# Optimization experiments

Measured on AMD Instinct MI355X. Metric: run time of the kernel, lower is better.

The kernel has to match this reference:

```python
import jax, jax.numpy as jnp
import numpy as np

EPS = 1e-5

def setup_inputs() -> dict:
    key = jax.random.key(0)
    kx, kq, kp = jax.random.split(key, 3)
    B, T, d = 4, 4096, 512
    x = jax.random.normal(kx, (B, T, d), dtype=jnp.float32)
    mask = jnp.tril(jnp.ones((T, T), dtype=jnp.int32))  # causal 0/1 mask
    gamma = jnp.ones((d,), dtype=jnp.float32)
    beta = jnp.zeros((d,), dtype=jnp.float32)
    Wqkv = jax.random.normal(kq, (d, 3 * d), dtype=jnp.float32) / np.sqrt(d)
    Wproj = jax.random.normal(kp, (d, d), dtype=jnp.float32) / np.sqrt(d)
    return {"x": x, "mask": mask, "gamma": gamma, "beta": beta, "Wqkv": Wqkv, "Wproj": Wproj}

def reference(x, mask, gamma, beta, Wqkv, Wproj):
    B, T, C = x.shape
    # LayerNorm over last dim
    mu = jnp.mean(x, axis=-1, keepdims=True)
    var = jnp.mean(jnp.square(x - mu), axis=-1, keepdims=True)
    xn = (x - mu) * jax.lax.rsqrt(var + EPS) * gamma + beta
    # QKV projection (no bias)
    qkv = xn @ Wqkv  # [B,T,3C]
    q, k, v = jnp.split(qkv, 3, axis=-1)
    scale = 1.0 / np.sqrt(C)
    dist = jnp.einsum('btc,bsc->bts', q, k) * scale  # [B,T,T]
    dist = jnp.where(mask[:T, :T] == 0, -jnp.inf, dist)
    attn = jax.nn.softmax(dist, axis=-1)
    out = jnp.einsum('bts,bsc->btc', attn, v)
    return out @ Wproj
```

## Files before the change

kernel.cpp:

```cpp
#include <hip/hip_runtime.h>

typedef short bf16x8 __attribute__((ext_vector_type(8)));
typedef float f32x4 __attribute__((ext_vector_type(4)));

#define AS1 __attribute__((address_space(1)))
#define AS3 __attribute__((address_space(3)))

__device__ __forceinline__ void async16(const void* g, void* l) {
    __builtin_amdgcn_global_load_lds((AS1 unsigned*)(unsigned long long)g,
                                     (AS3 unsigned*)l, 16, 0, 0);
}

__device__ __forceinline__ unsigned short f2bf(float f) {
    unsigned u = __builtin_bit_cast(unsigned, f);
    u += 0x7fffu + ((u >> 16) & 1u);
    return (unsigned short)(u >> 16);
}
__device__ __forceinline__ float bf2f(unsigned short s) {
    unsigned u = ((unsigned)s) << 16;
    return __builtin_bit_cast(float, u);
}

__global__ __launch_bounds__(256) void ln_bf16_kernel(
    const float* __restrict__ x, const float* __restrict__ gamma,
    const float* __restrict__ beta, unsigned short* __restrict__ xn, int nrows)
{
    int row = blockIdx.x * 4 + (threadIdx.x >> 6);
    int lane = threadIdx.x & 63;
    if (row >= nrows) return;
    const float4* xr = (const float4*)(x + (size_t)row * 512);
    float4 a = xr[lane], b = xr[lane + 64];
    float s = a.x + a.y + a.z + a.w + b.x + b.y + b.z + b.w;
    #pragma unroll
    for (int m = 1; m < 64; m <<= 1) s += __shfl_xor(s, m);
    float mu = s * (1.0f / 512.0f);
    float dx[8] = {a.x - mu, a.y - mu, a.z - mu, a.w - mu,
                   b.x - mu, b.y - mu, b.z - mu, b.w - mu};
    float ss = 0.f;
    #pragma unroll
    for (int i = 0; i < 8; ++i) ss += dx[i] * dx[i];
    #pragma unroll
    for (int m = 1; m < 64; m <<= 1) ss += __shfl_xor(ss, m);
    float rstd = rsqrtf(ss * (1.0f / 512.0f) + 1e-5f);
    const float4* gp = (const float4*)gamma;
    const float4* bp = (const float4*)beta;
    float4 g0 = gp[lane], g1 = gp[lane + 64], b0 = bp[lane], b1 = bp[lane + 64];
    float y[8];
    y[0] = dx[0] * rstd * g0.x + b0.x; y[1] = dx[1] * rstd * g0.y + b0.y;
    y[2] = dx[2] * rstd * g0.z + b0.z; y[3] = dx[3] * rstd * g0.w + b0.w;
    y[4] = dx[4] * rstd * g1.x + b1.x; y[5] = dx[5] * rstd * g1.y + b1.y;
    y[6] = dx[6] * rstd * g1.z + b1.z; y[7] = dx[7] * rstd * g1.w + b1.w;
    ushort4* orow = (ushort4*)(xn + (size_t)row * 512);
    orow[lane]      = make_ushort4(f2bf(y[0]), f2bf(y[1]), f2bf(y[2]), f2bf(y[3]));
    orow[lane + 64] = make_ushort4(f2bf(y[4]), f2bf(y[5]), f2bf(y[6]), f2bf(y[7]));
}

__global__ __launch_bounds__(256) void transpose_w(
    const float* __restrict__ in, unsigned short* __restrict__ outT, int R, int Cd)
{
    __shared__ float tile[64][65];
    int r0 = blockIdx.x * 64, c0 = blockIdx.y * 64;
    int lr = threadIdx.x >> 6, lc = threadIdx.x & 63;
    #pragma unroll
    for (int i = 0; i < 16; ++i) {
        int r = i * 4 + lr;
        tile[r][lc] = in[(size_t)(r0 + r) * Cd + c0 + lc];
    }
    __syncthreads();
    #pragma unroll
    for (int i = 0; i < 16; ++i) {
        int r = i * 4 + lr;
        outT[(size_t)(c0 + r) * R + r0 + lc] = f2bf(tile[lc][r]);
    }
}

__global__ __launch_bounds__(256) void transpose_v(
    const unsigned short* __restrict__ vraw, unsigned short* __restrict__ vtp)
{
    __shared__ unsigned short tile[64][72];
    int b = blockIdx.z;
    int t0 = blockIdx.x * 64, c0 = blockIdx.y * 64;
    int lr = threadIdx.x >> 6, lc = threadIdx.x & 63;
    const unsigned short* src = vraw + (size_t)(b * 4096 + t0) * 512 + c0;
    #pragma unroll
    for (int i = 0; i < 16; ++i) {
        int r = i * 4 + lr;
        tile[r][lc] = src[(size_t)r * 512 + lc];
    }
    __syncthreads();
    #pragma unroll
    for (int i = 0; i < 16; ++i) {
        int r = i * 4 + lr;
        int c = c0 + r;
        int jt = (t0 >> 5) + (lc >> 5);
        int tl = lc & 31;
        int x = tl >> 3;
        int slot = c * 4 + ((x ^ (c >> 1)) & 3);
        vtp[((size_t)(b * 128 + jt)) * 16384 + slot * 8 + (tl & 7)] = tile[lc][r];
    }
}

__global__ __launch_bounds__(256) void gemm_bt(
    const unsigned short* __restrict__ A, const unsigned short* __restrict__ Bt,
    void* __restrict__ Cp, int M, int N, int K, int lda, int ldb, int ldc, int outBf16)
{
    __shared__ unsigned short As[128 * 64];
    __shared__ unsigned short Bs[128 * 64];
    const int tid = threadIdx.x;
    const int w = tid >> 6, lane = tid & 63, quad = lane >> 4, l15 = lane & 15;
    const int wm = w >> 1, wn = w & 1;
    const size_t m0 = (size_t)blockIdx.x * 128, n0 = (size_t)blockIdx.y * 128;
    f32x4 zero = {0.f, 0.f, 0.f, 0.f};
    f32x4 acc[4][4];
    #pragma unroll
    for (int i = 0; i < 4; ++i)
        #pragma unroll
        for (int j = 0; j < 4; ++j) acc[i][j] = zero;

    for (int k0 = 0; k0 < K; k0 += 64) {
        __syncthreads();
        #pragma unroll
        for (int r = 0; r < 4; ++r) {
            int s = r * 256 + w * 64 + lane;
            int row = s >> 3, x = s & 7, g = x ^ (row & 7);
            async16(A + (m0 + row) * lda + k0 + g * 8,
                    (char*)As + (size_t)(r * 256 + w * 64) * 16);
        }
        #pragma unroll
        for (int r = 0; r < 4; ++r) {
            int s = r * 256 + w * 64 + lane;
            int row = s >> 3, x = s & 7, g = x ^ (row & 7);
            async16(Bt + (n0 + row) * ldb + k0 + g * 8,
                    (char*)Bs + (size_t)(r * 256 + w * 64) * 16);
        }
        __syncthreads();
        #pragma unroll
        for (int ks = 0; ks < 2; ++ks) {
            bf16x8 af[4], bf[4];
            int cc = ks * 4 + quad;
            #pragma unroll
            for (int mt = 0; mt < 4; ++mt) {
                int row = wm * 64 + mt * 16 + l15;
                int x = cc ^ (row & 7);
                af[mt] = *(const bf16x8*)(As + row * 64 + x * 8);
            }
            #pragma unroll
            for (int nt = 0; nt < 4; ++nt) {
                int row = wn * 64 + nt * 16 + l15;
                int x = cc ^ (row & 7);
                bf[nt] = *(const bf16x8*)(Bs + row * 64 + x * 8);
            }
            #pragma unroll
            for (int mt = 0; mt < 4; ++mt)
                #pragma unroll
                for (int nt = 0; nt < 4; ++nt)
                    acc[mt][nt] = __builtin_amdgcn_mfma_f32_16x16x32_bf16(
                        af[mt], bf[nt], acc[mt][nt], 0, 0, 0);
        }
    }
    #pragma unroll
    for (int mt = 0; mt < 4; ++mt)
        #pragma unroll
        for (int nt = 0; nt < 4; ++nt)
            #pragma unroll
            for (int r = 0; r < 4; ++r) {
                size_t grow = m0 + wm * 64 + mt * 16 + quad * 4 + r;
                size_t gcol = n0 + wn * 64 + nt * 16 + l15;
                float v = acc[mt][nt][r];
                if (outBf16) ((unsigned short*)Cp)[grow * ldc + gcol] = f2bf(v);
                else         ((float*)Cp)[grow * ldc + gcol] = v;
            }
}

__global__ __launch_bounds__(256, 2) void attn_kernel(
    const unsigned short* __restrict__ qk,
    const unsigned short* __restrict__ vtp,
    unsigned short* __restrict__ ph0, unsigned short* __restrict__ ph1,
    float* __restrict__ lp)
{
    __shared__ unsigned short Ks[32 * 512];
    __shared__ unsigned short Vs[32 * 512];
    __shared__ unsigned short Ps[64 * 40];

    const int id = blockIdx.x;
    const int cu = id & 255, hi = id >> 8;
    const int b = cu & 3;
    const int q = hi ? (63 - (cu >> 2)) : (cu >> 2);
    const int h = hi;

    const int jt0 = h ? (q + 1) : 0;
    const int jtN = h ? (2 * q + 2) : (q + 1);

    const int tid = threadIdx.x, w = tid >> 6, lane = tid & 63;
    const int quad = lane >> 4, l15 = lane & 15;
    const float scale = 0.04419417382415922f;
    f32x4 zero = {0.f, 0.f, 0.f, 0.f};

    const unsigned short* kbase = qk + (size_t)(b * 4096) * 1024 + 512;
    const unsigned short* vbase = vtp + (size_t)(b * 128) * 16384;
    unsigned short* dst = h ? ph1 : ph0;

    const int gE = (lane & ~7) | ((lane ^ w) & 7);
    const int gO = (lane & ~7) | ((lane ^ (w + 4)) & 7);
    const size_t kOffE = (size_t)w * 1024 + (size_t)gE * 8;
    const size_t kOffO = (size_t)(w + 4) * 1024 + (size_t)gO * 8;
    const size_t vOff  = (size_t)tid * 8;

    bf16x8 qf[16];
    {
        const unsigned short* qb =
            qk + (size_t)(b * 4096 + q * 64 + w * 16 + l15) * 1024;
        #pragma unroll
        for (int ks = 0; ks < 16; ++ks)
            qf[ks] = *(const bf16x8*)(qb + ks * 32 + quad * 8);
    }
    f32x4 o[4][8];
    #pragma unroll
    for (int i = 0; i < 4; ++i)
        #pragma unroll
        for (int d = 0; d < 8; ++d) o[i][d] = zero;
    float li[4] = {0.f, 0.f, 0.f, 0.f};

    for (int jt = jt0; jt < jtN; ++jt) {
        __syncthreads();
        {
            const unsigned short* kg = kbase + (size_t)jt * 32768;
            #pragma unroll
            for (int rr = 0; rr < 4; ++rr) {
                async16(kg + (size_t)(2 * rr) * 4096 + kOffE,
                        (char*)Ks + (size_t)((2 * rr) * 256 + w * 64) * 16);
                async16(kg + (size_t)(2 * rr) * 4096 + kOffO,
                        (char*)Ks + (size_t)((2 * rr + 1) * 256 + w * 64) * 16);
            }
            const unsigned short* vg = vbase + (size_t)jt * 16384 + vOff;
            #pragma unroll
            for (int rnd = 0; rnd < 8; ++rnd)
                async16(vg + (size_t)rnd * 2048,
                        (char*)Vs + (size_t)(rnd * 256 + w * 64) * 16);
        }
        __syncthreads();

        f32x4 sa[2];
        sa[0] = zero; sa[1] = zero;
        #pragma unroll
        for (int ks = 0; ks < 16; ++ks) {
            int cc = ks * 4 + quad;
            #pragma unroll
            for (int nt = 0; nt < 2; ++nt) {
                int jr = nt * 16 + l15;
                int xg = (cc & ~7) | ((cc ^ jr) & 7);
                bf16x8 kf = *(const bf16x8*)(Ks + jr * 512 + xg * 8);
                sa[nt] = __builtin_amdgcn_mfma_f32_16x16x32_bf16(
                    qf[ks], kf, sa[nt], 0, 0, 0);
            }
        }
        const int trow = q * 64 + w * 16 + quad * 4;
        #pragma unroll
        for (int r = 0; r < 4; ++r) {
            #pragma unroll
            for (int nt = 0; nt < 2; ++nt) {
                int col = jt * 32 + nt * 16 + l15;
                float sv = sa[nt][r] * scale;
                float pv = __expf(fminf(sv, 60.f));
                if (col > trow + r) pv = 0.f;
                li[r] += pv;
                Ps[(w * 16 + quad * 4 + r) * 40 + nt * 16 + l15] = f2bf(pv);
            }
        }
        asm volatile("s_waitcnt lgkmcnt(0)" ::: "memory");
        __builtin_amdgcn_s_barrier();

        #pragma unroll
        for (int ph = 0; ph < 2; ++ph) {
            bf16x8 vfr[4];
            #pragma unroll
            for (int d4 = 0; d4 < 4; ++d4) {
                int cch = (w * 8 + ph * 4 + d4) * 16 + l15;
                int slot = cch * 4 + ((quad ^ (cch >> 1)) & 3);
                vfr[d4] = *(const bf16x8*)(Vs + slot * 8);
            }
            #pragma unroll
            for (int qi = 0; qi < 4; ++qi) {
                bf16x8 pa = *(const bf16x8*)(Ps + (qi * 16 + l15) * 40 + quad * 8);
                #pragma unroll
                for (int d4 = 0; d4 < 4; ++d4)
                    o[qi][ph * 4 + d4] = __builtin_amdgcn_mfma_f32_16x16x32_bf16(
                        pa, vfr[d4], o[qi][ph * 4 + d4], 0, 0, 0);
            }
        }
    }

    #pragma unroll
    for (int r = 0; r < 4; ++r) {
        float s = li[r];
        s += __shfl_xor(s, 1);
        s += __shfl_xor(s, 2);
        s += __shfl_xor(s, 4);
        s += __shfl_xor(s, 8);
        if (l15 == 0)
            lp[h * 16384 + b * 4096 + q * 64 + w * 16 + quad * 4 + r] = s;
    }
    unsigned short* ob = dst + (size_t)(b * 4096 + q * 64) * 512 + w * 128;
    #pragma unroll
    for (int qi = 0; qi < 4; ++qi)
        #pragma unroll
        for (int df = 0; df < 8; ++df)
            #pragma unroll
            for (int r = 0; r < 4; ++r)
                ob[(size_t)(qi * 16 + quad * 4 + r) * 512 + df * 16 + l15] =
                    f2bf(o[qi][df][r]);
}

__global__ __launch_bounds__(256) void combine_kernel(
    const unsigned short* __restrict__ ph0, const unsigned short* __restrict__ ph1,
    const float* __restrict__ lp, unsigned short* __restrict__ att)
{
    int t = blockIdx.x * 4 + (threadIdx.x >> 6);
    int lane = threadIdx.x & 63;
    float inv = 1.0f / (lp[t] + lp[16384 + t]);
    const ushort4* pa = (const ushort4*)(ph0 + (size_t)t * 512 + lane * 8);
    const ushort4* pb = (const ushort4*)(ph1 + (size_t)t * 512 + lane * 8);
    ushort4* po = (ushort4*)(att + (size_t)t * 512 + lane * 8);
    #pragma unroll
    for (int i = 0; i < 2; ++i) {
        ushort4 a = pa[i], b = pb[i];
        po[i] = make_ushort4(
            f2bf((bf2f(a.x) + bf2f(b.x)) * inv),
            f2bf((bf2f(a.y) + bf2f(b.y)) * inv),
            f2bf((bf2f(a.z) + bf2f(b.z)) * inv),
            f2bf((bf2f(a.w) + bf2f(b.w)) * inv));
    }
}

extern "C" void kernel_launch(void* const* d_in, const int* in_sizes, int n_in,
                              void* d_out, int out_size, void* d_ws, size_t ws_size,
                              hipStream_t stream)
{
    const float* x     = (const float*)d_in[0];
    const float* gamma = (const float*)d_in[2];
    const float* beta  = (const float*)d_in[3];
    const float* Wqkv  = (const float*)d_in[4];
    const float* Wproj = (const float*)d_in[5];
    float* out = (float*)d_out;

    char* ws = (char*)d_ws;
    unsigned short* qk     = (unsigned short*)(ws);
    unsigned short* vraw   = (unsigned short*)(ws + 33554432);
    unsigned short* vtp    = (unsigned short*)(ws + 50331648);
    unsigned short* xn     = (unsigned short*)(ws + 67108864);
    unsigned short* wqkvT  = (unsigned short*)(ws + 83886080);
    unsigned short* wprojT = (unsigned short*)(ws + 85458944);
    unsigned short* ph0    = xn;
    unsigned short* ph1    = vraw;
    float*          lp     = (float*)wqkvT;
    unsigned short* att    = vtp;

    ln_bf16_kernel<<<4096, 256, 0, stream>>>(x, gamma, beta, xn, 16384);
    transpose_w<<<dim3(8, 24), 256, 0, stream>>>(Wqkv, wqkvT, 512, 1536);
    transpose_w<<<dim3(8, 8), 256, 0, stream>>>(Wproj, wprojT, 512, 512);
    gemm_bt<<<dim3(128, 8), 256, 0, stream>>>(xn, wqkvT, qk,
                                              16384, 1024, 512, 512, 512, 1024, 1);
    gemm_bt<<<dim3(128, 4), 256, 0, stream>>>(xn, wqkvT + 1024 * 512, vraw,
                                              16384, 512, 512, 512, 512, 512, 1);
    transpose_v<<<dim3(64, 8, 4), 256, 0, stream>>>(vraw, vtp);
    attn_kernel<<<512, 256, 0, stream>>>(qk, vtp, ph0, ph1, lp);
    combine_kernel<<<4096, 256, 0, stream>>>(ph0, ph1, lp, att);
    gemm_bt<<<dim3(128, 4), 256, 0, stream>>>(att, wprojT, out,
                                              16384, 512, 512, 512, 512, 512, 0);
}
```

Measured before the change: 362.6 us.

## Fuse QKV GEMMs and V transpose into one kernel; raise wave priority around MFMAs

Merges the two QKV projection GEMM launches into a single 128x12 grid. The V-part blocks write their output directly in the swizzled transposed layout the attention kernel expects, which removes the separate transpose_v kernel and its bf16 round trip through global memory. It also wraps the attention MFMA loops in s_setprio(1)/s_setprio(0) to favour waves issuing matrix ops. The cost is scattered 2-byte stores in the V epilogue, which may coalesce poorly.

```diff
diff --git a/kernel.cpp b/kernel.cpp
--- a/kernel.cpp
+++ b/kernel.cpp
@@ -74,35 +74,9 @@
     }
 }
 
-__global__ __launch_bounds__(256) void transpose_v(
-    const unsigned short* __restrict__ vraw, unsigned short* __restrict__ vtp)
-{
-    __shared__ unsigned short tile[64][72];
-    int b = blockIdx.z;
-    int t0 = blockIdx.x * 64, c0 = blockIdx.y * 64;
-    int lr = threadIdx.x >> 6, lc = threadIdx.x & 63;
-    const unsigned short* src = vraw + (size_t)(b * 4096 + t0) * 512 + c0;
-    #pragma unroll
-    for (int i = 0; i < 16; ++i) {
-        int r = i * 4 + lr;
-        tile[r][lc] = src[(size_t)r * 512 + lc];
-    }
-    __syncthreads();
-    #pragma unroll
-    for (int i = 0; i < 16; ++i) {
-        int r = i * 4 + lr;
-        int c = c0 + r;
-        int jt = (t0 >> 5) + (lc >> 5);
-        int tl = lc & 31;
-        int x = tl >> 3;
-        int slot = c * 4 + ((x ^ (c >> 1)) & 3);
-        vtp[((size_t)(b * 128 + jt)) * 16384 + slot * 8 + (tl & 7)] = tile[lc][r];
-    }
-}
-
-__global__ __launch_bounds__(256) void gemm_bt(
+__global__ __launch_bounds__(256) void gemm_qkv(
     const unsigned short* __restrict__ A, const unsigned short* __restrict__ Bt,
-    void* __restrict__ Cp, int M, int N, int K, int lda, int ldb, int ldc, int outBf16)
+    unsigned short* __restrict__ qkOut, unsigned short* __restrict__ vtp)
 {
     __shared__ unsigned short As[128 * 64];
     __shared__ unsigned short Bs[128 * 64];
@@ -117,6 +91,95 @@
         #pragma unroll
         for (int j = 0; j < 4; ++j) acc[i][j] = zero;
 
+    for (int k0 = 0; k0 < 512; k0 += 64) {
+        __syncthreads();
+        #pragma unroll
+        for (int r = 0; r < 4; ++r) {
+            int s = r * 256 + w * 64 + lane;
+            int row = s >> 3, x = s & 7, g = x ^ (row & 7);
+            async16(A + (m0 + row) * 512 + k0 + g * 8,
+                    (char*)As + (size_t)(r * 256 + w * 64) * 16);
+        }
+        #pragma unroll
+        for (int r = 0; r < 4; ++r) {
+            int s = r * 256 + w * 64 + lane;
+            int row = s >> 3, x = s & 7, g = x ^ (row & 7);
+            async16(Bt + (n0 + row) * 512 + k0 + g * 8,
+                    (char*)Bs + (size_t)(r * 256 + w * 64) * 16);
+        }
+        __syncthreads();
+        #pragma unroll
+        for (int ks = 0; ks < 2; ++ks) {
+            bf16x8 af[4], bf[4];
+            int cc = ks * 4 + quad;
+            #pragma unroll
+            for (int mt = 0; mt < 4; ++mt) {
+                int row = wm * 64 + mt * 16 + l15;
+                int x = cc ^ (row & 7);
+                af[mt] = *(const bf16x8*)(As + row * 64 + x * 8);
+            }
+            #pragma unroll
+            for (int nt = 0; nt < 4; ++nt) {
+                int row = wn * 64 + nt * 16 + l15;
+                int x = cc ^ (row & 7);
+                bf[nt] = *(const bf16x8*)(Bs + row * 64 + x * 8);
+            }
+            #pragma unroll
+            for (int mt = 0; mt < 4; ++mt)
+                #pragma unroll
+                for (int nt = 0; nt < 4; ++nt)
+                    acc[mt][nt] = __builtin_amdgcn_mfma_f32_16x16x32_bf16(
+                        af[mt], bf[nt], acc[mt][nt], 0, 0, 0);
+        }
+    }
+    if (n0 < 1024) {
+        #pragma unroll
+        for (int mt = 0; mt < 4; ++mt)
+            #pragma unroll
+            for (int nt = 0; nt < 4; ++nt)
+                #pragma unroll
+                for (int r = 0; r < 4; ++r) {
+                    size_t grow = m0 + wm * 64 + mt * 16 + quad * 4 + r;
+                    size_t gcol = n0 + wn * 64 + nt * 16 + l15;
+                    qkOut[grow * 1024 + gcol] = f2bf(acc[mt][nt][r]);
+                }
+    } else {
+        const int b = (int)(m0 >> 12);
+        const int tb = (int)(m0 & 4095);
+        #pragma unroll
+        for (int mt = 0; mt < 4; ++mt)
+            #pragma unroll
+            for (int nt = 0; nt < 4; ++nt)
+                #pragma unroll
+                for (int r = 0; r < 4; ++r) {
+                    int t = tb + wm * 64 + mt * 16 + quad * 4 + r;
+                    int vcol = (int)(n0 - 1024) + wn * 64 + nt * 16 + l15;
+                    int jt = t >> 5;
+                    int x = (t >> 3) & 3;
+                    int slot = vcol * 4 + ((x ^ (vcol >> 1)) & 3);
+                    vtp[(size_t)(b * 128 + jt) * 16384 + slot * 8 + (t & 7)] =
+                        f2bf(acc[mt][nt][r]);
+                }
+    }
+}
+
+__global__ __launch_bounds__(256) void gemm_bt(
+    const unsigned short* __restrict__ A, const unsigned short* __restrict__ Bt,
+    void* __restrict__ Cp, int M, int N, int K, int lda, int ldb, int ldc, int outBf16)
+{
+    __shared__ unsigned short As[128 * 64];
+    __shared__ unsigned short Bs[128 * 64];
+    const int tid = threadIdx.x;
+    const int w = tid >> 6, lane = tid & 63, quad = lane >> 4, l15 = lane & 15;
+    const int wm = w >> 1, wn = w & 1;
+    const size_t m0 = (size_t)blockIdx.x * 128, n0 = (size_t)blockIdx.y * 128;
+    f32x4 zero = {0.f, 0.f, 0.f, 0.f};
+    f32x4 acc[4][4];
+    #pragma unroll
+    for (int i = 0; i < 4; ++i)
+        #pragma unroll
+        for (int j = 0; j < 4; ++j) acc[i][j] = zero;
+
     for (int k0 = 0; k0 < K; k0 += 64) {
         __syncthreads();
         #pragma unroll
@@ -242,6 +305,7 @@
 
         f32x4 sa[2];
         sa[0] = zero; sa[1] = zero;
+        __builtin_amdgcn_s_setprio(1);
         #pragma unroll
         for (int ks = 0; ks < 16; ++ks) {
             int cc = ks * 4 + quad;
@@ -254,6 +318,7 @@
                     qf[ks], kf, sa[nt], 0, 0, 0);
             }
         }
+        __builtin_amdgcn_s_setprio(0);
         const int trow = q * 64 + w * 16 + quad * 4;
         #pragma unroll
         for (int r = 0; r < 4; ++r) {
@@ -270,6 +335,7 @@
         asm volatile("s_waitcnt lgkmcnt(0)" ::: "memory");
         __builtin_amdgcn_s_barrier();
 
+        __builtin_amdgcn_s_setprio(1);
         #pragma unroll
         for (int ph = 0; ph < 2; ++ph) {
             bf16x8 vfr[4];
@@ -288,6 +354,7 @@
                         pa, vfr[d4], o[qi][ph * 4 + d4], 0, 0, 0);
             }
         }
+        __builtin_amdgcn_s_setprio(0);
     }
 
     #pragma unroll
@@ -345,24 +412,19 @@
 
     char* ws = (char*)d_ws;
     unsigned short* qk     = (unsigned short*)(ws);
-    unsigned short* vraw   = (unsigned short*)(ws + 33554432);
+    unsigned short* ph1    = (unsigned short*)(ws + 33554432);
     unsigned short* vtp    = (unsigned short*)(ws + 50331648);
     unsigned short* xn     = (unsigned short*)(ws + 67108864);
     unsigned short* wqkvT  = (unsigned short*)(ws + 83886080);
     unsigned short* wprojT = (unsigned short*)(ws + 85458944);
     unsigned short* ph0    = xn;
-    unsigned short* ph1    = vraw;
     float*          lp     = (float*)wqkvT;
     unsigned short* att    = vtp;
 
     ln_bf16_kernel<<<4096, 256, 0, stream>>>(x, gamma, beta, xn, 16384);
     transpose_w<<<dim3(8, 24), 256, 0, stream>>>(Wqkv, wqkvT, 512, 1536);
     transpose_w<<<dim3(8, 8), 256, 0, stream>>>(Wproj, wprojT, 512, 512);
-    gemm_bt<<<dim3(128, 8), 256, 0, stream>>>(xn, wqkvT, qk,
-                                              16384, 1024, 512, 512, 512, 1024, 1);
-    gemm_bt<<<dim3(128, 4), 256, 0, stream>>>(xn, wqkvT + 1024 * 512, vraw,
-                                              16384, 512, 512, 512, 512, 512, 1);
-    transpose_v<<<dim3(64, 8, 4), 256, 0, stream>>>(vraw, vtp);
+    gemm_qkv<<<dim3(128, 12), 256, 0, stream>>>(xn, wqkvT, qk, vtp);
     attn_kernel<<<512, 256, 0, stream>>>(qk, vtp, ph0, ph1, lp);
     combine_kernel<<<4096, 256, 0, stream>>>(ph0, ph1, lp, att);
     gemm_bt<<<dim3(128, 4), 256, 0, stream>>>(att, wprojT, out,
```

Measured after the change: 351.0 us. -3.2%, faster.
